# Performance work log

Measured on AMD Instinct MI355X. Metric: run time of the kernel, lower is better.

The kernel has to match this reference:

```python
import jax, jax.numpy as jnp
import numpy as np

N_NODES = 50000
D_IN = 128
D_OUT = 128
E_POS = 500000
E_NEG = 100000
BN_EPS = 1e-5


def setup_inputs() -> dict:
    key = jax.random.key(0)
    k = jax.random.split(key, 4)
    x = jax.random.normal(k[0], (N_NODES, D_IN), dtype=jnp.float32)
    pos_edge_index = jax.random.randint(k[1], (2, E_POS), 0, N_NODES, dtype=jnp.int64)
    neg_edge_index = jax.random.randint(k[2], (2, E_NEG), 0, N_NODES, dtype=jnp.int64)
    W = jax.random.normal(k[3], (D_IN, D_OUT), dtype=jnp.float32) * 0.05
    b = jnp.zeros((D_OUT,), dtype=jnp.float32)
    gamma = jnp.ones((D_OUT,), dtype=jnp.float32)
    beta = jnp.zeros((D_OUT,), dtype=jnp.float32)
    return {"x": x, "pos_edge_index": pos_edge_index, "neg_edge_index": neg_edge_index,
            "W": W, "b": b, "gamma": gamma, "beta": beta}


def reference(x, pos_edge_index, neg_edge_index, W, b, gamma, beta):
    N = x.shape[0]
    # edge weights: 1 for pos edges, 0 for neg edges (as in the torch module)
    ei = jnp.concatenate([pos_edge_index, neg_edge_index], axis=1)
    w = jnp.concatenate([jnp.ones((pos_edge_index.shape[1],), x.dtype),
                         jnp.zeros((neg_edge_index.shape[1],), x.dtype)])
    # GCNConv gcn_norm: add self-loops with weight 1.0
    loop = jnp.arange(N)
    row = jnp.concatenate([ei[0], loop])
    col = jnp.concatenate([ei[1], loop])
    w = jnp.concatenate([w, jnp.ones((N,), x.dtype)])
    # symmetric degree normalization over target (col)
    deg = jax.ops.segment_sum(w, col, num_segments=N)
    dis = jnp.where(deg > 0, jax.lax.rsqrt(jnp.maximum(deg, 1e-12)), 0.0)
    norm = dis[row] * w * dis[col]  # [E_total]
    # linear transform first, then scatter-add aggregation at col
    h = x @ W  # [N, D_OUT]
    out = jax.ops.segment_sum(norm[:, None] * h[row], col, num_segments=N) + b
    # BatchNorm1d (training mode, biased batch var) + ReLU
    mean = out.mean(axis=0)
    var = out.var(axis=0)
    xhat = (out - mean) * jax.lax.rsqrt(var + BN_EPS)
    return jax.nn.relu(gamma * xhat + beta)
```

## Files before the change

kernel.cpp:

```cpp
#include <hip/hip_runtime.h>

#define D 128
#define BN_EPS 1e-5f
#define K_ELL 40
#define NB_AGG 1024
#define NB_FILL 1024

typedef __attribute__((ext_vector_type(8))) short bf16x8;
typedef __attribute__((ext_vector_type(4))) float f32x4;

__device__ __forceinline__ unsigned bf16rne(float f) {
    unsigned u = __float_as_uint(f);
    return (u + 0x7fffu + ((u >> 16) & 1u)) >> 16;
}
__device__ __forceinline__ float bflo(unsigned p) { return __uint_as_float(p << 16); }
__device__ __forceinline__ float bfhi(unsigned p) { return __uint_as_float(p & 0xffff0000u); }

__global__ __launch_bounds__(256) void gemm_fill(
    const float* __restrict__ x, const float* __restrict__ W,
    const int* __restrict__ prow, const int* __restrict__ pcol,
    int* __restrict__ deg, int* __restrict__ ell,
    int2* __restrict__ ovf, int* __restrict__ ovf_cnt,
    ushort* __restrict__ hb, int n, int E, int gemm_nb)
{
    __shared__ ushort xsb[64][136];
    __shared__ ushort wsb[128][136];
    int tid = threadIdx.x;

    if (blockIdx.x >= gemm_nb) {
        int gtid = (blockIdx.x - gemm_nb) * 256 + tid;
        for (int e = gtid; e < E; e += NB_FILL * 256) {
            int c = pcol[e];
            int r = prow[e];
            int p = atomicAdd(&deg[c], 1);
            if (p < K_ELL) {
                ell[c * K_ELL + p] = r;
            } else {
                int q = atomicAdd(ovf_cnt, 1);
                ovf[q] = make_int2(c, r);
            }
        }
        return;
    }

    int wave = tid >> 6;
    int lane = tid & 63;
    int row0 = blockIdx.x * 64;

    #pragma unroll
    for (int i = 0; i < 16; i++) {
        int flat = i * 256 + tid;
        int k = flat >> 5;
        int c4 = flat & 31;
        float4 v = *(const float4*)&W[k * D + c4 * 4];
        wsb[c4 * 4 + 0][k] = (ushort)bf16rne(v.x);
        wsb[c4 * 4 + 1][k] = (ushort)bf16rne(v.y);
        wsb[c4 * 4 + 2][k] = (ushort)bf16rne(v.z);
        wsb[c4 * 4 + 3][k] = (ushort)bf16rne(v.w);
    }
    {
        int r = tid >> 2, kq = tid & 3;
        int grow = row0 + r;
        if (grow >= n) grow = n - 1;
        const float4* src = (const float4*)&x[(size_t)grow * D + kq * 32];
        uint* dst = (uint*)&xsb[r][kq * 32];
        #pragma unroll
        for (int q = 0; q < 8; q++) {
            float4 v = src[q];
            dst[q * 2]     = bf16rne(v.x) | (bf16rne(v.y) << 16);
            dst[q * 2 + 1] = bf16rne(v.z) | (bf16rne(v.w) << 16);
        }
    }
    __syncthreads();

    f32x4 acc[4][2];
    #pragma unroll
    for (int mt = 0; mt < 4; mt++)
        #pragma unroll
        for (int nt = 0; nt < 2; nt++)
            acc[mt][nt] = (f32x4){0.f, 0.f, 0.f, 0.f};

    int ar = lane & 15;
    int ako = (lane >> 4) * 8;
    #pragma unroll
    for (int k0 = 0; k0 < 128; k0 += 32) {
        bf16x8 a[4], b[2];
        #pragma unroll
        for (int mt = 0; mt < 4; mt++)
            a[mt] = *(const bf16x8*)&xsb[mt * 16 + ar][k0 + ako];
        #pragma unroll
        for (int nt = 0; nt < 2; nt++)
            b[nt] = *(const bf16x8*)&wsb[wave * 32 + nt * 16 + ar][k0 + ako];
        #pragma unroll
        for (int mt = 0; mt < 4; mt++)
            #pragma unroll
            for (int nt = 0; nt < 2; nt++)
                acc[mt][nt] = __builtin_amdgcn_mfma_f32_16x16x32_bf16(
                    a[mt], b[nt], acc[mt][nt], 0, 0, 0);
    }

    int col = lane & 15, rq = (lane >> 4) * 4;
    #pragma unroll
    for (int mt = 0; mt < 4; mt++) {
        #pragma unroll
        for (int r = 0; r < 4; r++) {
            int grow = row0 + mt * 16 + rq + r;
            if (grow < n) {
                #pragma unroll
                for (int nt = 0; nt < 2; nt++)
                    hb[(size_t)grow * D + wave * 32 + nt * 16 + col] =
                        (ushort)bf16rne(acc[mt][nt][r]);
            }
        }
    }
}

__global__ __launch_bounds__(512) void aggregate(const unsigned* __restrict__ hb,
                                                 const int* __restrict__ deg,
                                                 const int* __restrict__ ell,
                                                 const int2* __restrict__ ovf,
                                                 const int* __restrict__ ovf_cnt,
                                                 const float* __restrict__ bias,
                                                 float* __restrict__ out,
                                                 float* __restrict__ partials, int n) {
    int tid = threadIdx.x;
    int wave = tid >> 6;
    int lane = tid & 63;
    float2 bv = *(const float2*)&bias[lane * 2];
    float s1a = 0.f, s1b = 0.f, s2a = 0.f, s2b = 0.f;

    for (int node = blockIdx.x * 8 + wave; node < n; node += gridDim.x * 8) {
        int cntT = deg[node];
        float dc = rsqrtf((float)cntT + 1.0f);
        int cntE = cntT < K_ELL ? cntT : K_ELL;
        unsigned hp = hb[(size_t)node * 64 + lane];
        float ax = dc * bflo(hp), ay = dc * bfhi(hp);
        int es = (lane < cntE) ? ell[node * K_ELL + lane] : 0;
        float ed = (lane < cntE) ? rsqrtf((float)deg[es] + 1.0f) : 0.f;
        int e = 0;
        for (; e + 4 <= cntE; e += 4) {
            int sA = __shfl(es, e), sB = __shfl(es, e + 1);
            int sC = __shfl(es, e + 2), sD = __shfl(es, e + 3);
            float dA = __shfl(ed, e), dB = __shfl(ed, e + 1);
            float dC = __shfl(ed, e + 2), dD = __shfl(ed, e + 3);
            unsigned hA = hb[(size_t)sA * 64 + lane];
            unsigned hB = hb[(size_t)sB * 64 + lane];
            unsigned hC = hb[(size_t)sC * 64 + lane];
            unsigned hD = hb[(size_t)sD * 64 + lane];
            ax += dA * bflo(hA); ay += dA * bfhi(hA);
            ax += dB * bflo(hB); ay += dB * bfhi(hB);
            ax += dC * bflo(hC); ay += dC * bfhi(hC);
            ax += dD * bflo(hD); ay += dD * bfhi(hD);
        }
        for (; e < cntE; e++) {
            int s = __shfl(es, e);
            float dv = __shfl(ed, e);
            unsigned hq = hb[(size_t)s * 64 + lane];
            ax += dv * bflo(hq); ay += dv * bfhi(hq);
        }
        if (cntT > K_ELL) {
            int novf = *ovf_cnt;
            for (int j = 0; j < novf; j++) {
                int2 q = ovf[j];
                if (q.x == node) {
                    float dv = rsqrtf((float)deg[q.y] + 1.0f);
                    unsigned hq = hb[(size_t)q.y * 64 + lane];
                    ax += dv * bflo(hq); ay += dv * bfhi(hq);
                }
            }
        }
        float ox = dc * ax + bv.x;
        float oy = dc * ay + bv.y;
        *(float2*)&out[(size_t)node * D + lane * 2] = make_float2(ox, oy);
        s1a += ox; s1b += oy;
        s2a += ox * ox; s2b += oy * oy;
    }

    __shared__ float l1[8][128], l2[8][128];
    l1[wave][lane * 2] = s1a; l1[wave][lane * 2 + 1] = s1b;
    l2[wave][lane * 2] = s2a; l2[wave][lane * 2 + 1] = s2b;
    __syncthreads();
    if (tid < 256) {
        int col = tid & 127;
        float v;
        if (tid < 128) {
            v = l1[0][col] + l1[1][col] + l1[2][col] + l1[3][col] +
                l1[4][col] + l1[5][col] + l1[6][col] + l1[7][col];
        } else {
            v = l2[0][col] + l2[1][col] + l2[2][col] + l2[3][col] +
                l2[4][col] + l2[5][col] + l2[6][col] + l2[7][col];
        }
        partials[(size_t)blockIdx.x * 256 + tid] = v;
    }
}

__global__ __launch_bounds__(256) void bn_reduce(const float* __restrict__ partials,
                                                 float* __restrict__ gsum,
                                                 float* __restrict__ gsumsq, int nrows) {
    int tid = threadIdx.x;
    float s = 0.f;
    for (int r = blockIdx.x; r < nrows; r += gridDim.x)
        s += partials[(size_t)r * 256 + tid];
    if (tid < 128) atomicAdd(&gsum[tid], s);
    else           atomicAdd(&gsumsq[tid - 128], s);
}

__global__ __launch_bounds__(256) void bn_finalize(float4* __restrict__ out4,
                                                   const float* __restrict__ gsum,
                                                   const float* __restrict__ gsumsq,
                                                   const float* __restrict__ gamma,
                                                   const float* __restrict__ beta,
                                                   int total4, float invN) {
    int i0 = blockIdx.x * 256 + threadIdx.x;
    int c = (i0 * 4) & 127;
    float4 g4 = *(const float4*)&gsum[c];
    float4 q4 = *(const float4*)&gsumsq[c];
    float4 gm = *(const float4*)&gamma[c];
    float4 bt = *(const float4*)&beta[c];
    float m0 = g4.x * invN, m1 = g4.y * invN, m2 = g4.z * invN, m3 = g4.w * invN;
    float sc0 = rsqrtf(q4.x * invN - m0 * m0 + BN_EPS) * gm.x;
    float sc1 = rsqrtf(q4.y * invN - m1 * m1 + BN_EPS) * gm.y;
    float sc2 = rsqrtf(q4.z * invN - m2 * m2 + BN_EPS) * gm.z;
    float sc3 = rsqrtf(q4.w * invN - m3 * m3 + BN_EPS) * gm.w;
    float sh0 = bt.x - m0 * sc0, sh1 = bt.y - m1 * sc1;
    float sh2 = bt.z - m2 * sc2, sh3 = bt.w - m3 * sc3;
    for (int i = i0; i < total4; i += gridDim.x * 256) {
        float4 v = out4[i];
        v.x = fmaxf(fmaf(v.x, sc0, sh0), 0.f);
        v.y = fmaxf(fmaf(v.y, sc1, sh1), 0.f);
        v.z = fmaxf(fmaf(v.z, sc2, sh2), 0.f);
        v.w = fmaxf(fmaf(v.w, sc3, sh3), 0.f);
        out4[i] = v;
    }
}

extern "C" void kernel_launch(void* const* d_in, const int* in_sizes, int n_in,
                              void* d_out, int out_size, void* d_ws, size_t ws_size,
                              hipStream_t stream) {
    const float* x     = (const float*)d_in[0];
    const int*   pos   = (const int*)d_in[1];
    const float* W     = (const float*)d_in[3];
    const float* bias  = (const float*)d_in[4];
    const float* gamma = (const float*)d_in[5];
    const float* beta  = (const float*)d_in[6];
    float* out = (float*)d_out;

    int N  = in_sizes[0] / D;
    int EP = in_sizes[1] / 2;
    const int* prow = pos;
    const int* pcol = pos + EP;
    int gemm_nb = (N + 63) / 64;

    auto align = [](size_t v) { return (v + 255) & ~(size_t)255; };
    char* p = (char*)d_ws;
    int*    deg     = (int*)p;    p += align((size_t)N * 4);
    int*    ovf_cnt = (int*)p;    p += align(256);
    float*  gsum    = (float*)p;  p += align((size_t)D * 4);
    float*  gsumsq  = (float*)p;  p += align((size_t)D * 4);
    size_t zbytes = (size_t)(p - (char*)d_ws);
    int*    ell      = (int*)p;    p += align((size_t)N * K_ELL * 4);
    int2*   ovf      = (int2*)p;   p += align((size_t)EP * 8);
    ushort* hb       = (ushort*)p; p += align((size_t)N * D * 2);
    float*  partials = (float*)p;  p += align((size_t)NB_AGG * 256 * 4);

    hipMemsetAsync(d_ws, 0, zbytes, stream);
    gemm_fill<<<gemm_nb + NB_FILL, 256, 0, stream>>>(x, W, prow, pcol, deg, ell, ovf,
                                                     ovf_cnt, hb, N, EP, gemm_nb);
    aggregate<<<NB_AGG, 512, 0, stream>>>((const unsigned*)hb, deg, ell, ovf, ovf_cnt,
                                          bias, out, partials, N);
    bn_reduce<<<64, 256, 0, stream>>>(partials, gsum, gsumsq, NB_AGG);
    bn_finalize<<<1600, 256, 0, stream>>>((float4*)out, gsum, gsumsq, gamma, beta,
                                          N * D / 4, 1.0f / (float)N);
}
```

Baseline: 164.1 us.

## Load W fragments directly into registers and double aggregation grid size

```diff
diff --git a/kernel.cpp b/kernel.cpp
--- a/kernel.cpp
+++ b/kernel.cpp
@@ -3,7 +3,7 @@
 #define D 128
 #define BN_EPS 1e-5f
 #define K_ELL 40
-#define NB_AGG 1024
+#define NB_AGG 2048
 #define NB_FILL 1024
 
 typedef __attribute__((ext_vector_type(8))) short bf16x8;
@@ -24,7 +24,6 @@
     ushort* __restrict__ hb, int n, int E, int gemm_nb)
 {
     __shared__ ushort xsb[64][136];
-    __shared__ ushort wsb[128][136];
     int tid = threadIdx.x;
 
     if (blockIdx.x >= gemm_nb) {
@@ -46,18 +45,26 @@
     int wave = tid >> 6;
     int lane = tid & 63;
     int row0 = blockIdx.x * 64;
-
-    #pragma unroll
-    for (int i = 0; i < 16; i++) {
-        int flat = i * 256 + tid;
-        int k = flat >> 5;
-        int c4 = flat & 31;
-        float4 v = *(const float4*)&W[k * D + c4 * 4];
-        wsb[c4 * 4 + 0][k] = (ushort)bf16rne(v.x);
-        wsb[c4 * 4 + 1][k] = (ushort)bf16rne(v.y);
-        wsb[c4 * 4 + 2][k] = (ushort)bf16rne(v.z);
-        wsb[c4 * 4 + 3][k] = (ushort)bf16rne(v.w);
-    }
+    int ar = lane & 15;
+    int ako = (lane >> 4) * 8;
+
+    bf16x8 bfrag[4][2];
+    #pragma unroll
+    for (int kk = 0; kk < 4; kk++) {
+        #pragma unroll
+        for (int nt = 0; nt < 2; nt++) {
+            const float* wp = &W[(kk * 32 + ako) * D + wave * 32 + nt * 16 + ar];
+            uint bu[4];
+            #pragma unroll
+            for (int j = 0; j < 4; j++) {
+                float f0 = wp[(2 * j) * D];
+                float f1 = wp[(2 * j + 1) * D];
+                bu[j] = bf16rne(f0) | (bf16rne(f1) << 16);
+            }
+            bfrag[kk][nt] = *(bf16x8*)bu;
+        }
+    }
+
     {
         int r = tid >> 2, kq = tid & 3;
         int grow = row0 + r;
@@ -80,23 +87,18 @@
         for (int nt = 0; nt < 2; nt++)
             acc[mt][nt] = (f32x4){0.f, 0.f, 0.f, 0.f};
 
-    int ar = lane & 15;
-    int ako = (lane >> 4) * 8;
-    #pragma unroll
-    for (int k0 = 0; k0 < 128; k0 += 32) {
-        bf16x8 a[4], b[2];
+    #pragma unroll
+    for (int kk = 0; kk < 4; kk++) {
+        bf16x8 a[4];
         #pragma unroll
         for (int mt = 0; mt < 4; mt++)
-            a[mt] = *(const bf16x8*)&xsb[mt * 16 + ar][k0 + ako];
-        #pragma unroll
-        for (int nt = 0; nt < 2; nt++)
-            b[nt] = *(const bf16x8*)&wsb[wave * 32 + nt * 16 + ar][k0 + ako];
+            a[mt] = *(const bf16x8*)&xsb[mt * 16 + ar][kk * 32 + ako];
         #pragma unroll
         for (int mt = 0; mt < 4; mt++)
             #pragma unroll
             for (int nt = 0; nt < 2; nt++)
                 acc[mt][nt] = __builtin_amdgcn_mfma_f32_16x16x32_bf16(
-                    a[mt], b[nt], acc[mt][nt], 0, 0, 0);
+                    a[mt], bfrag[kk][nt], acc[mt][nt], 0, 0, 0);
     }
 
     int col = lane & 15, rq = (lane >> 4) * 4;
```

New measurement: 176.4 us. +7.5%, slower.
